# Kernel optimization log

Measured on AMD Instinct MI355X. Metric: run time of the kernel, lower is better.

Reference implementation:

```python
import jax, jax.numpy as jnp
import numpy as np

N = 50000      # nodes
E = 800000     # edges (avg degree 16)
D_IN = 128
H = 128
D_OUT = 64
L = 3          # num GCNConv layers


def setup_inputs() -> dict:
    key = jax.random.key(0)
    ks = jax.random.split(key, 9)
    x = jax.random.normal(ks[0], (N, D_IN), jnp.float32)
    edge_index = jax.random.randint(ks[1], (2, E), 0, N, dtype=jnp.int32)
    s_in = 1.0 / np.sqrt(D_IN)
    s_h = 1.0 / np.sqrt(H)
    W1 = jax.random.normal(ks[2], (D_IN, H), jnp.float32) * s_in
    b1 = jnp.zeros((H,), jnp.float32)
    Wc = jax.random.normal(ks[3], (L, H, H), jnp.float32) * s_h
    bc = jnp.zeros((L, H), jnp.float32)
    W2 = jax.random.normal(ks[4], (H, D_OUT), jnp.float32) * s_h
    b2 = jnp.zeros((D_OUT,), jnp.float32)
    return {"x": x, "edge_index": edge_index, "W1": W1, "b1": b1,
            "Wc": Wc, "bc": bc, "W2": W2, "b2": b2}


def reference(x, edge_index, W1, b1, Wc, bc, W2, b2):
    n = x.shape[0]
    src, dst = edge_index[0], edge_index[1]
    # GCNConv normalization with self-loops: deg[i] = 1 + in-degree(i)
    deg = jnp.zeros((n,), x.dtype).at[dst].add(1.0) + 1.0
    dis = jax.lax.rsqrt(deg)                       # D^{-1/2}
    norm = dis[src] * dis[dst]                     # per-edge norm, [E]
    self_norm = (dis * dis)[:, None]               # self-loop norm, [n,1]
    # dnn1: Linear + ReLU
    h = jax.nn.relu(x @ W1 + b1)
    # GCNConv layers: x' = D^{-1/2}(A+I)D^{-1/2} X W + b
    for l in range(Wc.shape[0]):
        hw = h @ Wc[l]                             # [n, H]
        msg = hw[src] * norm[:, None]              # gather + scale, [E, H]
        agg = jax.ops.segment_sum(msg, dst, num_segments=n)
        h = agg + self_norm * hw + bc[l]
    # dnn2: Linear
    return h @ W2 + b2
```

## Files before the change

kernel.cpp:

```cpp
#include <hip/hip_runtime.h>
#include <hip/hip_fp16.h>


typedef _Float16 f16;
typedef __attribute__((ext_vector_type(8))) _Float16 f16x8;
typedef __attribute__((ext_vector_type(4))) float f32x4;

constexpr int H = 128;
constexpr int CH = 512;


__global__ __launch_bounds__(256) void k_degree_cvtw(const int* __restrict__ dst,
                                                     int* __restrict__ cnt,
                                                     int* __restrict__ rank, int E, int EB,
                                                     const float* __restrict__ W1,
                                                     const float* __restrict__ Wc,
                                                     const float* __restrict__ W2,
                                                     f16* __restrict__ BT1,
                                                     f16* __restrict__ BTc,
                                                     f16* __restrict__ BT2) {
    if (blockIdx.x < (unsigned)EB) {
        int e = blockIdx.x * 256 + threadIdx.x;
        if (e < E) rank[e] = atomicAdd(&cnt[dst[e]], 1);
    } else {
        int i = (blockIdx.x - EB) * 256 + threadIdx.x;
        if (i < 16384) {
            int c = i >> 7, k = i & 127;
            BT1[i] = (f16)W1[k * 128 + c];
        } else if (i < 65536) {
            int j = i - 16384;
            int l = j >> 14, r = j & 16383;
            int c = r >> 7, k = r & 127;
            BTc[j] = (f16)Wc[l * 16384 + k * 128 + c];
        } else if (i < 73728) {
            int j = i - 65536;
            int c = j >> 7, k = j & 127;
            BT2[j] = (f16)W2[k * 64 + c];
        }
    }
}

__global__ __launch_bounds__(CH) void k_scan1(const int* __restrict__ cnt,
                                              int* __restrict__ roff,
                                              int* __restrict__ csum,
                                              float* __restrict__ dis,
                                              float* __restrict__ dis2, int n) {
    __shared__ int sh[CH];
    int t = threadIdx.x;
    int i = blockIdx.x * CH + t;
    int v = (i < n) ? cnt[i] : 0;
    if (i < n) {
        float r = rsqrtf((float)(v + 1));
        dis[i] = r;
        dis2[i] = r * r;
    }
    int pd = (v + 7) & ~7;
    sh[t] = pd;
    __syncthreads();
    for (int off = 1; off < CH; off <<= 1) {
        int x = (t >= off) ? sh[t - off] : 0;
        __syncthreads();
        sh[t] += x;
        __syncthreads();
    }
    if (i < n) roff[i] = sh[t] - pd;
    if (t == CH - 1) csum[blockIdx.x] = sh[t];
}

__global__ __launch_bounds__(256) void k_scan2(const int* __restrict__ csum,
                                               int* __restrict__ coff,
                                               int* __restrict__ roff, int n, int nch) {
    __shared__ int sh[256];
    int t = threadIdx.x;
    int v = (t < nch) ? csum[t] : 0;
    sh[t] = v;
    __syncthreads();
    for (int off = 1; off < 256; off <<= 1) {
        int x = (t >= off) ? sh[t - off] : 0;
        __syncthreads();
        sh[t] += x;
        __syncthreads();
    }
    if (t < nch) coff[t] = sh[t] - v;
    if (t == nch - 1) roff[n] = sh[t];
}

__global__ __launch_bounds__(256) void k_scan3(int* __restrict__ roff,
                                               const int* __restrict__ coff, int n) {
    int i = blockIdx.x * 256 + threadIdx.x;
    if (i < n) roff[i] += coff[i / CH];
}

__global__ __launch_bounds__(256) void k_fill(const int* __restrict__ src,
                                              const int* __restrict__ dst,
                                              const int* __restrict__ rank,
                                              const int* __restrict__ roff,
                                              const float* __restrict__ dis,
                                              unsigned long long* __restrict__ edata,
                                              int E) {
    int e = blockIdx.x * 256 + threadIdx.x;
    if (e < E) {
        int d = dst[e], s = src[e];
        int pos = roff[d] + rank[e];
        float nm = dis[s] * dis[d];
        unsigned long long v = (unsigned long long)(unsigned)s |
                               ((unsigned long long)__float_as_uint(nm) << 32);
        atomicExch(&edata[pos], v);
    }
}


template <int NCOLS, int MODE, bool AF32>
__global__ __launch_bounds__(256) void k_gemm16(const void* __restrict__ Av,
                                                const f16* __restrict__ BT,
                                                const float* __restrict__ bias,
                                                void* __restrict__ Cv, int n) {
    constexpr int CT = NCOLS / 16;
    constexpr int BSTR = H + 8;
    __shared__ f16 Bs[NCOLS * BSTR];

    const int tid = threadIdx.x;
    constexpr int CHUNKS = NCOLS * H / (256 * 8);
#pragma unroll
    for (int it = 0; it < CHUNKS; ++it) {
        int idx = tid + it * 256;
        int r = idx >> 4;
        int c8 = idx & 15;
        *(f16x8*)&Bs[r * BSTR + c8 * 8] = *(const f16x8*)&BT[r * H + c8 * 8];
    }
    __syncthreads();

    const int l = tid & 63;
    const int w = tid >> 6;
    const int lrow = l & 15;
    const int lk = (l >> 4) * 8;
    int arow = blockIdx.x * 64 + w * 16 + lrow;
    int arc = arow < n ? arow : n - 1;

    f16x8 a[4];
    if constexpr (AF32) {
        const float* ap = (const float*)Av + (size_t)arc * H;
#pragma unroll
        for (int ks = 0; ks < 4; ++ks) {
            float4 u = *(const float4*)&ap[ks * 32 + lk];
            float4 v = *(const float4*)&ap[ks * 32 + lk + 4];
            f16x8 t;
            t[0] = (f16)u.x; t[1] = (f16)u.y; t[2] = (f16)u.z; t[3] = (f16)u.w;
            t[4] = (f16)v.x; t[5] = (f16)v.y; t[6] = (f16)v.z; t[7] = (f16)v.w;
            a[ks] = t;
        }
    } else {
        const f16* ap = (const f16*)Av + (size_t)arc * H;
#pragma unroll
        for (int ks = 0; ks < 4; ++ks) a[ks] = *(const f16x8*)&ap[ks * 32 + lk];
    }

    f32x4 acc[CT];
#pragma unroll
    for (int ct = 0; ct < CT; ++ct) acc[ct] = (f32x4)(0.f);

#pragma unroll
    for (int ks = 0; ks < 4; ++ks) {
#pragma unroll
        for (int ct = 0; ct < CT; ++ct) {
            f16x8 b = *(const f16x8*)&Bs[(ct * 16 + lrow) * BSTR + ks * 32 + lk];
            acc[ct] = __builtin_amdgcn_mfma_f32_16x16x32_f16(a[ks], b, acc[ct], 0, 0, 0);
        }
    }

    const int rbase = blockIdx.x * 64 + w * 16 + (l >> 4) * 4;
#pragma unroll
    for (int ct = 0; ct < CT; ++ct) {
        int col = ct * 16 + lrow;
        float bv = 0.f;
        if constexpr (MODE != 0) bv = bias[col];
#pragma unroll
        for (int r = 0; r < 4; ++r) {
            int row = rbase + r;
            if (row >= n) continue;
            float v = acc[ct][r] + bv;
            if constexpr (MODE == 1) v = fmaxf(v, 0.f);
            if constexpr (MODE == 2)
                ((float*)Cv)[(size_t)row * NCOLS + col] = v;
            else
                ((f16*)Cv)[(size_t)row * NCOLS + col] = (f16)v;
        }
    }
}


__global__ __launch_bounds__(512) void k_agg16(const __half2* __restrict__ hw,
                                               const int* __restrict__ roff,
                                               const long long* __restrict__ edata,
                                               const float* __restrict__ dis2,
                                               const float* __restrict__ bias,
                                               unsigned int* __restrict__ hout, int n) {
    int wave = threadIdx.x >> 6;
    int lane = threadIdx.x & 63;
    int node = blockIdx.x * 8 + wave;
    if (node >= n) return;

    int e = roff[node];
    const int e1 = roff[node + 1];

    float2 sv = __half22float2(hw[(size_t)node * 64 + lane]);
    float d2 = dis2[node];
    float ax = sv.x * d2, ay = sv.y * d2;

    long long cur[8], nxt[8];
    if (e < e1) {
#pragma unroll
        for (int j = 0; j < 8; ++j) cur[j] = edata[e + j];
    }
    while (e < e1) {
        int en = e + 8;
        if (en < e1) {
#pragma unroll
            for (int j = 0; j < 8; ++j) nxt[j] = edata[en + j];
        }
        float2 v[8];
#pragma unroll
        for (int j = 0; j < 8; ++j)
            v[j] = __half22float2(hw[(size_t)(unsigned)(cur[j] & 0xffffffff) * 64 + lane]);
#pragma unroll
        for (int j = 0; j < 8; ++j) {
            float nm = __int_as_float((int)(cur[j] >> 32));
            ax = fmaf(nm, v[j].x, ax);
            ay = fmaf(nm, v[j].y, ay);
        }
#pragma unroll
        for (int j = 0; j < 8; ++j) cur[j] = nxt[j];
        e = en;
    }

    float2 b = ((const float2*)bias)[lane];
    ax += b.x; ay += b.y;
    __half2 r = __float22half2_rn(make_float2(ax, ay));
    hout[(size_t)node * 64 + lane] = *(unsigned int*)&r;
}


extern "C" void kernel_launch(void* const* d_in, const int* in_sizes, int n_in,
                              void* d_out, int out_size, void* d_ws, size_t ws_size,
                              hipStream_t stream) {
    const float* x  = (const float*)d_in[0];
    const int*   ei = (const int*)d_in[1];
    const float* W1 = (const float*)d_in[2];
    const float* b1 = (const float*)d_in[3];
    const float* Wc = (const float*)d_in[4];
    const float* bc = (const float*)d_in[5];
    const float* W2 = (const float*)d_in[6];
    const float* b2 = (const float*)d_in[7];
    float* out = (float*)d_out;

    const int n = in_sizes[0] / H;
    const int E = in_sizes[1] / 2;
    const int* src = ei;
    const int* dst = ei + E;

    char* p = (char*)d_ws;
    auto alloc = [&](size_t b) -> void* {
        void* r = (void*)p;
        p += (b + 255) & ~(size_t)255;
        return r;
    };
    f16*   h    = (f16*)alloc((size_t)n * H * 2);
    f16*   hw   = (f16*)alloc((size_t)n * H * 2);
    f16*   BT1  = (f16*)alloc(16384 * 2);
    f16*   BTc  = (f16*)alloc(3 * 16384 * 2);
    f16*   BT2  = (f16*)alloc(8192 * 2);
    int*   cnt  = (int*)alloc((size_t)n * 4);
    int*   rank = (int*)alloc((size_t)E * 4);
    int*   roff = (int*)alloc((size_t)(n + 1) * 4);
    const int nch = (n + CH - 1) / CH;
    int*   csum = (int*)alloc((size_t)nch * 4);
    int*   coff = (int*)alloc((size_t)nch * 4);
    const size_t ecap = (size_t)E + 8 * (size_t)n;
    unsigned long long* edata = (unsigned long long*)alloc(ecap * 8);
    float* dis  = (float*)alloc((size_t)n * 4);
    float* dis2 = (float*)alloc((size_t)n * 4);

    hipMemsetAsync(cnt, 0, (size_t)n * 4, stream);
    hipMemsetAsync(edata, 0, ecap * 8, stream);

    const int EB = (E + 255) / 256;
    k_degree_cvtw<<<EB + 288, 256, 0, stream>>>(dst, cnt, rank, E, EB,
                                                W1, Wc, W2, BT1, BTc, BT2);
    k_scan1<<<nch, CH, 0, stream>>>(cnt, roff, csum, dis, dis2, n);
    k_scan2<<<1, 256, 0, stream>>>(csum, coff, roff, n, nch);
    k_scan3<<<(n + 255) / 256, 256, 0, stream>>>(roff, coff, n);
    k_fill<<<EB, 256, 0, stream>>>(src, dst, rank, roff, dis, edata, E);

    const int gblk = (n + 63) / 64;
    k_gemm16<128, 1, true><<<gblk, 256, 0, stream>>>(x, BT1, b1, h, n);
    for (int l = 0; l < 3; ++l) {
        k_gemm16<128, 0, false><<<gblk, 256, 0, stream>>>(h, BTc + (size_t)l * 16384, nullptr, hw, n);
        k_agg16<<<(n + 7) / 8, 512, 0, stream>>>((const __half2*)hw, roff, (const long long*)edata,
                                                 dis2, bc + (size_t)l * H, (unsigned int*)h, n);
    }
    k_gemm16<64, 2, false><<<gblk, 256, 0, stream>>>(h, BT2, b2, out, n);
}
```

Baseline: 319.1 us.

## Fuse aggregation with GEMM via (A·H)·W reordering and single-pass scan

Each GCN layer now aggregates neighbor features first and multiplies by the weight afterwards, inside one kernel. Each wave gathers 16 nodes into shared memory and then runs an MFMA GEMM on them. This removes the separate GEMM launch and the hw intermediate round-trip through global memory. The self-loop is written into the edge list as an extra entry carrying dis², and the three-kernel prefix scan becomes one kernel that gets each block's base from an atomic. In exchange, the block layout of edges becomes non-deterministic, and fp16 rounding of the aggregate before the GEMM may change accuracy.

```diff
diff --git a/kernel.cpp b/kernel.cpp
--- a/kernel.cpp
+++ b/kernel.cpp
@@ -7,7 +7,6 @@
 typedef __attribute__((ext_vector_type(4))) float f32x4;
 
 constexpr int H = 128;
-constexpr int CH = 512;
 
 
 __global__ __launch_bounds__(256) void k_degree_cvtw(const int* __restrict__ dst,
@@ -40,68 +39,50 @@
     }
 }
 
-__global__ __launch_bounds__(CH) void k_scan1(const int* __restrict__ cnt,
-                                              int* __restrict__ roff,
-                                              int* __restrict__ csum,
-                                              float* __restrict__ dis,
-                                              float* __restrict__ dis2, int n) {
-    __shared__ int sh[CH];
+__global__ __launch_bounds__(512) void k_scanA(const int* __restrict__ cnt,
+                                               int* __restrict__ gtot,
+                                               int2* __restrict__ roff2,
+                                               float* __restrict__ dis,
+                                               unsigned long long* __restrict__ edata,
+                                               int n, int n64) {
+    __shared__ int sh[512];
+    __shared__ int sbase;
     int t = threadIdx.x;
-    int i = blockIdx.x * CH + t;
-    int v = (i < n) ? cnt[i] : 0;
-    if (i < n) {
-        float r = rsqrtf((float)(v + 1));
-        dis[i] = r;
-        dis2[i] = r * r;
-    }
-    int pd = (v + 7) & ~7;
+    int i = blockIdx.x * 512 + t;
+    int c = (i < n) ? cnt[i] : 0;
+    int pd = (i < n64) ? ((c + 8) & ~7) : 0;
     sh[t] = pd;
     __syncthreads();
-    for (int off = 1; off < CH; off <<= 1) {
+    for (int off = 1; off < 512; off <<= 1) {
         int x = (t >= off) ? sh[t - off] : 0;
         __syncthreads();
         sh[t] += x;
         __syncthreads();
     }
-    if (i < n) roff[i] = sh[t] - pd;
-    if (t == CH - 1) csum[blockIdx.x] = sh[t];
-}
-
-__global__ __launch_bounds__(256) void k_scan2(const int* __restrict__ csum,
-                                               int* __restrict__ coff,
-                                               int* __restrict__ roff, int n, int nch) {
-    __shared__ int sh[256];
-    int t = threadIdx.x;
-    int v = (t < nch) ? csum[t] : 0;
-    sh[t] = v;
+    if (t == 511) sbase = atomicAdd(gtot, sh[511]);
     __syncthreads();
-    for (int off = 1; off < 256; off <<= 1) {
-        int x = (t >= off) ? sh[t - off] : 0;
-        __syncthreads();
-        sh[t] += x;
-        __syncthreads();
-    }
-    if (t < nch) coff[t] = sh[t] - v;
-    if (t == nch - 1) roff[n] = sh[t];
-}
-
-__global__ __launch_bounds__(256) void k_scan3(int* __restrict__ roff,
-                                               const int* __restrict__ coff, int n) {
-    int i = blockIdx.x * 256 + threadIdx.x;
-    if (i < n) roff[i] += coff[i / CH];
+    int off0 = sbase + sh[t] - pd;
+    if (i < n64) roff2[i] = make_int2(off0, pd);
+    if (i < n) {
+        float r = rsqrtf((float)(c + 1));
+        dis[i] = r;
+        unsigned long long sv = (unsigned long long)(unsigned)i |
+                                ((unsigned long long)__float_as_uint(r * r) << 32);
+        atomicExch(&edata[off0 + c], sv);
+    }
 }
 
 __global__ __launch_bounds__(256) void k_fill(const int* __restrict__ src,
                                               const int* __restrict__ dst,
                                               const int* __restrict__ rank,
-                                              const int* __restrict__ roff,
+                                              const int2* __restrict__ roff2,
                                               const float* __restrict__ dis,
                                               unsigned long long* __restrict__ edata,
                                               int E) {
     int e = blockIdx.x * 256 + threadIdx.x;
     if (e < E) {
         int d = dst[e], s = src[e];
-        int pos = roff[d] + rank[e];
+        int pos = roff2[d].x + rank[e];
         float nm = dis[s] * dis[d];
         unsigned long long v = (unsigned long long)(unsigned)s |
                                ((unsigned long long)__float_as_uint(nm) << 32);
@@ -172,8 +153,7 @@
 #pragma unroll
     for (int ct = 0; ct < CT; ++ct) {
         int col = ct * 16 + lrow;
-        float bv = 0.f;
-        if constexpr (MODE != 0) bv = bias[col];
+        float bv = bias[col];
 #pragma unroll
         for (int r = 0; r < 4; ++r) {
             int row = rbase + r;
@@ -189,54 +169,105 @@
 }
 
 
-__global__ __launch_bounds__(512) void k_agg16(const __half2* __restrict__ hw,
-                                               const int* __restrict__ roff,
-                                               const long long* __restrict__ edata,
-                                               const float* __restrict__ dis2,
-                                               const float* __restrict__ bias,
-                                               unsigned int* __restrict__ hout, int n) {
-    int wave = threadIdx.x >> 6;
-    int lane = threadIdx.x & 63;
-    int node = blockIdx.x * 8 + wave;
-    if (node >= n) return;
-
-    int e = roff[node];
-    const int e1 = roff[node + 1];
-
-    float2 sv = __half22float2(hw[(size_t)node * 64 + lane]);
-    float d2 = dis2[node];
-    float ax = sv.x * d2, ay = sv.y * d2;
+__global__ __launch_bounds__(256) void k_aggemm(const f16* __restrict__ hin,
+                                                const int2* __restrict__ roff2,
+                                                const long long* __restrict__ edata,
+                                                const f16* __restrict__ BT,
+                                                const float* __restrict__ bias,
+                                                f16* __restrict__ hout, int n) {
+    constexpr int BSTR = H + 8;
+    __shared__ f16 Bs[H * BSTR];
+    __shared__ f16 As[4][16 * BSTR];
+
+    const int tid = threadIdx.x;
+#pragma unroll
+    for (int it = 0; it < 8; ++it) {
+        int idx = tid + it * 256;
+        int r = idx >> 4, c8 = idx & 15;
+        *(f16x8*)&Bs[r * BSTR + c8 * 8] = *(const f16x8*)&BT[r * H + c8 * 8];
+    }
+
+    const int l = tid & 63;
+    const int w = tid >> 6;
+    const int first = blockIdx.x * 64 + w * 16;
+
+    int2 rj = roff2[first + (l & 15)];
+    int pdv = rj.y;
+    int e    = __shfl(rj.x, 0);
+    int eW   = __shfl(rj.x, 15) + __shfl(rj.y, 15);
+    int eend = e + __shfl(pdv, 0);
+
+    const __half2* h2 = (const __half2*)hin;
+    f16* Aw = As[w];
+
+    float ax = 0.f, ay = 0.f;
+    int j = 0;
 
     long long cur[8], nxt[8];
-    if (e < e1) {
-#pragma unroll
-        for (int j = 0; j < 8; ++j) cur[j] = edata[e + j];
-    }
-    while (e < e1) {
+    {
+        int es = __builtin_amdgcn_readfirstlane(e);
+#pragma unroll
+        for (int q = 0; q < 8; ++q) cur[q] = edata[es + q];
+    }
+    while (e < eW) {
         int en = e + 8;
-        if (en < e1) {
-#pragma unroll
-            for (int j = 0; j < 8; ++j) nxt[j] = edata[en + j];
+        if (en < eW) {
+            int es = __builtin_amdgcn_readfirstlane(en);
+#pragma unroll
+            for (int q = 0; q < 8; ++q) nxt[q] = edata[es + q];
         }
         float2 v[8];
 #pragma unroll
-        for (int j = 0; j < 8; ++j)
-            v[j] = __half22float2(hw[(size_t)(unsigned)(cur[j] & 0xffffffff) * 64 + lane]);
-#pragma unroll
-        for (int j = 0; j < 8; ++j) {
-            float nm = __int_as_float((int)(cur[j] >> 32));
-            ax = fmaf(nm, v[j].x, ax);
-            ay = fmaf(nm, v[j].y, ay);
-        }
-#pragma unroll
-        for (int j = 0; j < 8; ++j) cur[j] = nxt[j];
+        for (int q = 0; q < 8; ++q)
+            v[q] = __half22float2(h2[(size_t)(unsigned)(cur[q] & 0xffffffffLL) * 64 + l]);
+#pragma unroll
+        for (int q = 0; q < 8; ++q) {
+            float nm = __int_as_float((int)(cur[q] >> 32));
+            ax = fmaf(nm, v[q].x, ax);
+            ay = fmaf(nm, v[q].y, ay);
+        }
+#pragma unroll
+        for (int q = 0; q < 8; ++q) cur[q] = nxt[q];
         e = en;
-    }
-
-    float2 b = ((const float2*)bias)[lane];
-    ax += b.x; ay += b.y;
-    __half2 r = __float22half2_rn(make_float2(ax, ay));
-    hout[(size_t)node * 64 + lane] = *(unsigned int*)&r;
+        while (e >= eend && j < 16) {
+            __half2 hv = __float22half2_rn(make_float2(ax, ay));
+            *(__half2*)&Aw[j * BSTR + l * 2] = hv;
+            ax = 0.f; ay = 0.f;
+            ++j;
+            eend += __shfl(pdv, j < 16 ? j : 15);
+        }
+    }
+    __syncthreads();
+
+    const int lrow = l & 15;
+    const int lk = (l >> 4) * 8;
+    f16x8 a[4];
+#pragma unroll
+    for (int ks = 0; ks < 4; ++ks)
+        a[ks] = *(const f16x8*)&Aw[lrow * BSTR + ks * 32 + lk];
+
+    f32x4 acc[8];
+#pragma unroll
+    for (int ct = 0; ct < 8; ++ct) acc[ct] = (f32x4)(0.f);
+#pragma unroll
+    for (int ks = 0; ks < 4; ++ks)
+#pragma unroll
+        for (int ct = 0; ct < 8; ++ct) {
+            f16x8 b = *(const f16x8*)&Bs[(ct * 16 + lrow) * BSTR + ks * 32 + lk];
+            acc[ct] = __builtin_amdgcn_mfma_f32_16x16x32_f16(a[ks], b, acc[ct], 0, 0, 0);
+        }
+
+    const int rbase = first + (l >> 4) * 4;
+#pragma unroll
+    for (int ct = 0; ct < 8; ++ct) {
+        int col = ct * 16 + lrow;
+        float bv = bias[col];
+#pragma unroll
+        for (int r = 0; r < 4; ++r) {
+            int row = rbase + r;
+            if (row < n) hout[(size_t)row * H + col] = (f16)(acc[ct][r] + bv);
+        }
+    }
 }
 
 
@@ -255,6 +286,7 @@
 
     const int n = in_sizes[0] / H;
     const int E = in_sizes[1] / 2;
+    const int n64 = (n + 63) & ~63;
     const int* src = ei;
     const int* dst = ei + E;
 
@@ -264,39 +296,33 @@
         p += (b + 255) & ~(size_t)255;
         return r;
     };
-    f16*   h    = (f16*)alloc((size_t)n * H * 2);
-    f16*   hw   = (f16*)alloc((size_t)n * H * 2);
+    f16*   h    = (f16*)alloc((size_t)n64 * H * 2);
+    f16*   h2   = (f16*)alloc((size_t)n64 * H * 2);
     f16*   BT1  = (f16*)alloc(16384 * 2);
     f16*   BTc  = (f16*)alloc(3 * 16384 * 2);
     f16*   BT2  = (f16*)alloc(8192 * 2);
-    int*   cnt  = (int*)alloc((size_t)n * 4);
+    int*   cntg = (int*)alloc((size_t)(n + 1) * 4);
+    int*   cnt  = cntg;
+    int*   gtot = cntg + n;
     int*   rank = (int*)alloc((size_t)E * 4);
-    int*   roff = (int*)alloc((size_t)(n + 1) * 4);
-    const int nch = (n + CH - 1) / CH;
-    int*   csum = (int*)alloc((size_t)nch * 4);
-    int*   coff = (int*)alloc((size_t)nch * 4);
-    const size_t ecap = (size_t)E + 8 * (size_t)n;
+    int2*  roff2 = (int2*)alloc((size_t)n64 * 8);
+    const size_t ecap = (size_t)E + 8 * (size_t)n64;
     unsigned long long* edata = (unsigned long long*)alloc(ecap * 8);
     float* dis  = (float*)alloc((size_t)n * 4);
-    float* dis2 = (float*)alloc((size_t)n * 4);
-
-    hipMemsetAsync(cnt, 0, (size_t)n * 4, stream);
+
+    hipMemsetAsync(cntg, 0, (size_t)(n + 1) * 4, stream);
     hipMemsetAsync(edata, 0, ecap * 8, stream);
 
     const int EB = (E + 255) / 256;
     k_degree_cvtw<<<EB + 288, 256, 0, stream>>>(dst, cnt, rank, E, EB,
                                                 W1, Wc, W2, BT1, BTc, BT2);
-    k_scan1<<<nch, CH, 0, stream>>>(cnt, roff, csum, dis, dis2, n);
-    k_scan2<<<1, 256, 0, stream>>>(csum, coff, roff, n, nch);
-    k_scan3<<<(n + 255) / 256, 256, 0, stream>>>(roff, coff, n);
-    k_fill<<<EB, 256, 0, stream>>>(src, dst, rank, roff, dis, edata, E);
-
-    const int gblk = (n + 63) / 64;
+    k_scanA<<<(n64 + 511) / 512, 512, 0, stream>>>(cnt, gtot, roff2, dis, edata, n, n64);
+    k_fill<<<EB, 256, 0, stream>>>(src, dst, rank, roff2, dis, edata, E);
+
+    const int gblk = n64 / 64;
     k_gemm16<128, 1, true><<<gblk, 256, 0, stream>>>(x, BT1, b1, h, n);
-    for (int l = 0; l < 3; ++l) {
-        k_gemm16<128, 0, false><<<gblk, 256, 0, stream>>>(h, BTc + (size_t)l * 16384, nullptr, hw, n);
-        k_agg16<<<(n + 7) / 8, 512, 0, stream>>>((const __half2*)hw, roff, (const long long*)edata,
-                                                 dis2, bc + (size_t)l * H, (unsigned int*)h, n);
-    }
-    k_gemm16<64, 2, false><<<gblk, 256, 0, stream>>>(h, BT2, b2, out, n);
-}
+    k_aggemm<<<gblk, 256, 0, stream>>>(h,  roff2, (const long long*)edata, BTc,         bc,       h2, n);
+    k_aggemm<<<gblk, 256, 0, stream>>>(h2, roff2, (const long long*)edata, BTc + 16384, bc + 128, h,  n);
+    k_aggemm<<<gblk, 256, 0, stream>>>(h,  roff2, (const long long*)edata, BTc + 32768, bc + 256, h2, n);
+    k_gemm16<64, 2, false><<<gblk, 256, 0, stream>>>(h2, BT2, b2, out, n);
+}
```

New measurement: 424.7 us. 1.33x slower.
